# Optimization experiments

Hardware: AMD Instinct MI355X
Metric: run time of the kernel (lower is better)

## Reference

```python
import jax, jax.numpy as jnp
from jax import lax
import numpy as np


def setup_inputs() -> dict:
    key = jax.random.key(0)
    k1, k2, k3, k4 = jax.random.split(key, 4)
    H = W = 512
    N = 32
    return {
        "image": jax.random.normal(k1, (1, H, W), dtype=jnp.float32),
        "x": jax.random.normal(k2, (N, 1, H, W), dtype=jnp.float32),
        "KL_w": jax.random.normal(k3, (9, 1, 3, 3), dtype=jnp.float32) * 0.1,
        "KL_b": jax.random.normal(k4, (9,), dtype=jnp.float32) * 0.1,
    }


def reference(image, x, KL_w, KL_b):
    # Per-pixel 3x3 kernel generation: Conv2d(1 -> 9, 3x3, SAME) on the geometry image.
    # image: [1, H, W] (unbatched, 1 channel)
    K = lax.conv_general_dilated(
        image[None],              # [1, 1, H, W]
        KL_w,                     # [9, 1, 3, 3]
        window_strides=(1, 1),
        padding="SAME",
        dimension_numbers=("NCHW", "OIHW", "NCHW"),
    )[0] + KL_b[:, None, None]    # [9, H, W]
    H, W = K.shape[1], K.shape[2]
    Kp = jnp.transpose(K, (1, 2, 0))  # [H, W, 9]; channel c = 3*i + j (row-major 3x3)

    xs = x[:, 0]                               # [N, H, W]
    xp = jnp.pad(xs, ((0, 0), (1, 1), (1, 1)))  # zero pad, matches F.pad
    # Overlapping 3x3 patches as 9 shifted views, stacked row-major to match unfold order.
    patches = jnp.stack(
        [xp[:, i:i + H, j:j + W] for i in range(3) for j in range(3)], axis=-1
    )  # [N, H, W, 9]

    # Per-pixel FMA + reduce: y[n,h,w] = sum_k patches[n,h,w,k] * Kp[h,w,k]
    y = jnp.einsum("nhwk,hwk->nhw", patches, Kp)
    return y
```

## Files before the change

kernel.cpp:

```cpp
#include <hip/hip_runtime.h>

#define HH 512
#define WW 512
#define HWSZ (HH * WW)
#define NPB 4
#define RSTRIDE 520

__global__ __launch_bounds__(128) void fused_smblock(const float* __restrict__ img,
                                                     const float* __restrict__ x,
                                                     const float* __restrict__ kw,
                                                     const float* __restrict__ kb,
                                                     float* __restrict__ y) {
    __shared__ float rows[3][RSTRIDE];
    const int tid = threadIdx.x;
    const int h   = blockIdx.x;
    const int n0  = blockIdx.y * NPB;
    const int w4  = tid * 4;

    if (tid < 3) { rows[tid][3] = 0.0f; rows[tid][516] = 0.0f; }

    const bool vm1 = (h - 1) >= 0;
    const bool vp1 = (h + 1) < HH;

    {
        float4 r0 = vm1 ? *reinterpret_cast<const float4*>(img + (h - 1) * WW + w4) : make_float4(0, 0, 0, 0);
        float4 r1 =       *reinterpret_cast<const float4*>(img + h * WW + w4);
        float4 r2 = vp1 ? *reinterpret_cast<const float4*>(img + (h + 1) * WW + w4) : make_float4(0, 0, 0, 0);
        *reinterpret_cast<float4*>(&rows[0][w4 + 4]) = r0;
        *reinterpret_cast<float4*>(&rows[1][w4 + 4]) = r1;
        *reinterpret_cast<float4*>(&rows[2][w4 + 4]) = r2;
    }
    __syncthreads();

    float iv[3][6];
#pragma unroll
    for (int i = 0; i < 3; ++i) {
        float4 v = *reinterpret_cast<const float4*>(&rows[i][w4 + 4]);
        iv[i][0] = rows[i][w4 + 3];
        iv[i][1] = v.x; iv[i][2] = v.y; iv[i][3] = v.z; iv[i][4] = v.w;
        iv[i][5] = rows[i][w4 + 8];
    }

    float Kr[9][4];
#pragma unroll
    for (int c = 0; c < 9; ++c) {
        float b = kb[c];
#pragma unroll
        for (int p = 0; p < 4; ++p) Kr[c][p] = b;
#pragma unroll
        for (int i = 0; i < 3; ++i)
#pragma unroll
            for (int q = 0; q < 3; ++q) {
                float wv = kw[c * 9 + i * 3 + q];
#pragma unroll
                for (int p = 0; p < 4; ++p)
                    Kr[c][p] = fmaf(iv[i][p + q], wv, Kr[c][p]);
            }
    }
    __syncthreads();

    float4 pr[3];
    {
        const float* base = x + (size_t)n0 * HWSZ;
        pr[0] = vm1 ? *reinterpret_cast<const float4*>(base + (h - 1) * WW + w4) : make_float4(0, 0, 0, 0);
        pr[1] =       *reinterpret_cast<const float4*>(base + h * WW + w4);
        pr[2] = vp1 ? *reinterpret_cast<const float4*>(base + (h + 1) * WW + w4) : make_float4(0, 0, 0, 0);
    }

    for (int nn = 0; nn < NPB; ++nn) {
        *reinterpret_cast<float4*>(&rows[0][w4 + 4]) = pr[0];
        *reinterpret_cast<float4*>(&rows[1][w4 + 4]) = pr[1];
        *reinterpret_cast<float4*>(&rows[2][w4 + 4]) = pr[2];
        __syncthreads();

        if (nn + 1 < NPB) {
            const float* base = x + (size_t)(n0 + nn + 1) * HWSZ;
            pr[0] = vm1 ? *reinterpret_cast<const float4*>(base + (h - 1) * WW + w4) : make_float4(0, 0, 0, 0);
            pr[1] =       *reinterpret_cast<const float4*>(base + h * WW + w4);
            pr[2] = vp1 ? *reinterpret_cast<const float4*>(base + (h + 1) * WW + w4) : make_float4(0, 0, 0, 0);
        }

        float a[4] = {0, 0, 0, 0};
#pragma unroll
        for (int i = 0; i < 3; ++i) {
            float xv[6];
            float4 v = *reinterpret_cast<const float4*>(&rows[i][w4 + 4]);
            xv[0] = rows[i][w4 + 3];
            xv[1] = v.x; xv[2] = v.y; xv[3] = v.z; xv[4] = v.w;
            xv[5] = rows[i][w4 + 8];
#pragma unroll
            for (int j = 0; j < 3; ++j) {
                const int c = i * 3 + j;
#pragma unroll
                for (int p = 0; p < 4; ++p)
                    a[p] = fmaf(xv[p + j], Kr[c][p], a[p]);
            }
        }
        *reinterpret_cast<float4*>(&y[(size_t)(n0 + nn) * HWSZ + h * WW + w4]) =
            make_float4(a[0], a[1], a[2], a[3]);
        __syncthreads();
    }
}

extern "C" void kernel_launch(void* const* d_in, const int* in_sizes, int n_in,
                              void* d_out, int out_size, void* d_ws, size_t ws_size,
                              hipStream_t stream) {
    const float* img = (const float*)d_in[0];
    const float* x   = (const float*)d_in[1];
    const float* kw  = (const float*)d_in[2];
    const float* kb  = (const float*)d_in[3];
    float* y = (float*)d_out;

    dim3 grid(HH, 32 / NPB);
    fused_smblock<<<grid, 128, 0, stream>>>(img, x, kw, kb, y);
}
```

Before: 101.3 us.

## Pipeline x-plane loads into a triple-buffered LDS via direct global-to-LDS loads

Replaces register-staged prefetch of the three input rows with asynchronous global_load_lds transfers into a three-deep LDS ring, issuing two planes ahead. Hand-placed vmcnt waits and raw s_barriers take the place of __syncthreads. NPB doubles to 8, which halves the grid and raises per-block reuse of the generated kernel weights. The risks are fewer blocks to hide latency and fragile manual waitcnt counting, since the stores to y also count toward vmcnt. Out-of-range rows are redirected to a trash buffer.

```diff
diff --git a/kernel.cpp b/kernel.cpp
--- a/kernel.cpp
+++ b/kernel.cpp
@@ -1,52 +1,92 @@
 #include <hip/hip_runtime.h>
+#include <stdint.h>
 
 #define HH 512
 #define WW 512
 #define HWSZ (HH * WW)
-#define NPB 4
+#define NPB 8
 #define RSTRIDE 520
+#define NBUF 3
 
-__global__ __launch_bounds__(128) void fused_smblock(const float* __restrict__ img,
+__device__ __forceinline__ void gload16(const float* gsrc, float* ldst) {
+    __builtin_amdgcn_global_load_lds(
+        (const __attribute__((address_space(1))) void*)(uintptr_t)gsrc,
+        (__attribute__((address_space(3))) void*)(uint32_t)(uintptr_t)ldst,
+        16, 0, 0);
+}
+
+__global__ __launch_bounds__(128, 4) void fused_pipe(const float* __restrict__ img,
                                                      const float* __restrict__ x,
                                                      const float* __restrict__ kw,
                                                      const float* __restrict__ kb,
                                                      float* __restrict__ y) {
-    __shared__ float rows[3][RSTRIDE];
-    const int tid = threadIdx.x;
-    const int h   = blockIdx.x;
-    const int n0  = blockIdx.y * NPB;
-    const int w4  = tid * 4;
+    __shared__ float rows[NBUF][3][RSTRIDE];
+    __shared__ float trash[256];
 
-    if (tid < 3) { rows[tid][3] = 0.0f; rows[tid][516] = 0.0f; }
+    const int tid  = threadIdx.x;
+    const int h    = blockIdx.x;
+    const int n0   = blockIdx.y * NPB;
+    const int w4   = tid * 4;
+    const int wseg = (tid >> 6) * 256;
+    const bool vm1 = h > 0, vp1 = h < HH - 1;
 
-    const bool vm1 = (h - 1) >= 0;
-    const bool vp1 = (h + 1) < HH;
+    int  srcRow[3];
+    bool valid[3];
+    srcRow[0] = vm1 ? (h - 1) * WW : h * WW;  valid[0] = vm1;
+    srcRow[1] = h * WW;                       valid[1] = true;
+    srcRow[2] = vp1 ? (h + 1) * WW : h * WW;  valid[2] = vp1;
+
+    if (tid < NBUF * 3) {
+        rows[tid / 3][tid % 3][3]   = 0.0f;
+        rows[tid / 3][tid % 3][516] = 0.0f;
+    }
+    if (!vm1 || !vp1) {
+        const int bad = vm1 ? 2 : 0;
+        for (int s = tid; s < NBUF * 128; s += 128) {
+            int b = s >> 7, t = s & 127;
+            *reinterpret_cast<float4*>(&rows[b][bad][4 + t * 4]) = make_float4(0, 0, 0, 0);
+        }
+    }
 
     {
-        float4 r0 = vm1 ? *reinterpret_cast<const float4*>(img + (h - 1) * WW + w4) : make_float4(0, 0, 0, 0);
+        float4 z = make_float4(0, 0, 0, 0);
+        float4 r0 = vm1 ? *reinterpret_cast<const float4*>(img + (h - 1) * WW + w4) : z;
         float4 r1 =       *reinterpret_cast<const float4*>(img + h * WW + w4);
-        float4 r2 = vp1 ? *reinterpret_cast<const float4*>(img + (h + 1) * WW + w4) : make_float4(0, 0, 0, 0);
-        *reinterpret_cast<float4*>(&rows[0][w4 + 4]) = r0;
-        *reinterpret_cast<float4*>(&rows[1][w4 + 4]) = r1;
-        *reinterpret_cast<float4*>(&rows[2][w4 + 4]) = r2;
+        float4 r2 = vp1 ? *reinterpret_cast<const float4*>(img + (h + 1) * WW + w4) : z;
+        *reinterpret_cast<float4*>(&rows[0][0][4 + w4]) = r0;
+        *reinterpret_cast<float4*>(&rows[0][1][4 + w4]) = r1;
+        *reinterpret_cast<float4*>(&rows[0][2][4 + w4]) = r2;
     }
     __syncthreads();
 
     float iv[3][6];
 #pragma unroll
     for (int i = 0; i < 3; ++i) {
-        float4 v = *reinterpret_cast<const float4*>(&rows[i][w4 + 4]);
-        iv[i][0] = rows[i][w4 + 3];
+        float4 v = *reinterpret_cast<const float4*>(&rows[0][i][4 + w4]);
+        iv[i][0] = rows[0][i][3 + w4];
         iv[i][1] = v.x; iv[i][2] = v.y; iv[i][3] = v.z; iv[i][4] = v.w;
-        iv[i][5] = rows[i][w4 + 8];
+        iv[i][5] = rows[0][i][8 + w4];
     }
+
+    auto issue_plane = [&](int p) {
+        const float* xn = x + (size_t)(n0 + p) * HWSZ;
+        const int b = (p + 1) % 3;
+#pragma unroll
+        for (int i = 0; i < 3; ++i) {
+            const float* src = xn + srcRow[i] + tid * 4;
+            float* dst = valid[i] ? &rows[b][i][4 + wseg] : trash;
+            gload16(src, dst);
+        }
+    };
+    issue_plane(0);
+    issue_plane(1);
 
     float Kr[9][4];
 #pragma unroll
     for (int c = 0; c < 9; ++c) {
-        float b = kb[c];
+        float bv = kb[c];
 #pragma unroll
-        for (int p = 0; p < 4; ++p) Kr[c][p] = b;
+        for (int p = 0; p < 4; ++p) Kr[c][p] = bv;
 #pragma unroll
         for (int i = 0; i < 3; ++i)
 #pragma unroll
@@ -57,37 +97,31 @@
                     Kr[c][p] = fmaf(iv[i][p + q], wv, Kr[c][p]);
             }
     }
-    __syncthreads();
 
-    float4 pr[3];
-    {
-        const float* base = x + (size_t)n0 * HWSZ;
-        pr[0] = vm1 ? *reinterpret_cast<const float4*>(base + (h - 1) * WW + w4) : make_float4(0, 0, 0, 0);
-        pr[1] =       *reinterpret_cast<const float4*>(base + h * WW + w4);
-        pr[2] = vp1 ? *reinterpret_cast<const float4*>(base + (h + 1) * WW + w4) : make_float4(0, 0, 0, 0);
-    }
+    asm volatile("" ::: "memory");
+    __builtin_amdgcn_s_barrier();
+    __builtin_amdgcn_sched_barrier(0);
 
+#pragma unroll
     for (int nn = 0; nn < NPB; ++nn) {
-        *reinterpret_cast<float4*>(&rows[0][w4 + 4]) = pr[0];
-        *reinterpret_cast<float4*>(&rows[1][w4 + 4]) = pr[1];
-        *reinterpret_cast<float4*>(&rows[2][w4 + 4]) = pr[2];
-        __syncthreads();
+        if (nn + 2 < NPB) issue_plane(nn + 2);
 
-        if (nn + 1 < NPB) {
-            const float* base = x + (size_t)(n0 + nn + 1) * HWSZ;
-            pr[0] = vm1 ? *reinterpret_cast<const float4*>(base + (h - 1) * WW + w4) : make_float4(0, 0, 0, 0);
-            pr[1] =       *reinterpret_cast<const float4*>(base + h * WW + w4);
-            pr[2] = vp1 ? *reinterpret_cast<const float4*>(base + (h + 1) * WW + w4) : make_float4(0, 0, 0, 0);
-        }
+        if (nn == 0)              asm volatile("s_waitcnt vmcnt(6)" ::: "memory");
+        else if (nn < NPB - 2)    asm volatile("s_waitcnt vmcnt(7)" ::: "memory");
+        else if (nn == NPB - 2)   asm volatile("s_waitcnt vmcnt(4)" ::: "memory");
+        else                      asm volatile("s_waitcnt vmcnt(1)" ::: "memory");
+        __builtin_amdgcn_s_barrier();
+        __builtin_amdgcn_sched_barrier(0);
 
+        const int b = (nn + 1) % 3;
         float a[4] = {0, 0, 0, 0};
 #pragma unroll
         for (int i = 0; i < 3; ++i) {
             float xv[6];
-            float4 v = *reinterpret_cast<const float4*>(&rows[i][w4 + 4]);
-            xv[0] = rows[i][w4 + 3];
+            float4 v = *reinterpret_cast<const float4*>(&rows[b][i][4 + w4]);
+            xv[0] = rows[b][i][3 + w4];
             xv[1] = v.x; xv[2] = v.y; xv[3] = v.z; xv[4] = v.w;
-            xv[5] = rows[i][w4 + 8];
+            xv[5] = rows[b][i][8 + w4];
 #pragma unroll
             for (int j = 0; j < 3; ++j) {
                 const int c = i * 3 + j;
@@ -98,7 +132,10 @@
         }
         *reinterpret_cast<float4*>(&y[(size_t)(n0 + nn) * HWSZ + h * WW + w4]) =
             make_float4(a[0], a[1], a[2], a[3]);
-        __syncthreads();
+
+        __builtin_amdgcn_sched_barrier(0);
+        __builtin_amdgcn_s_barrier();
+        __builtin_amdgcn_sched_barrier(0);
     }
 }
 
@@ -112,5 +149,5 @@
     float* y = (float*)d_out;
 
     dim3 grid(HH, 32 / NPB);
-    fused_smblock<<<grid, 128, 0, stream>>>(img, x, kw, kb, y);
+    fused_pipe<<<grid, 128, 0, stream>>>(img, x, kw, kb, y);
 }
```

Result: no change. 103.1 us (+1.8%).
